# Optimization experiments

Hardware: AMD Instinct MI355X
Metric: run time of the kernel (lower is better)

## Reference

```python
import jax, jax.numpy as jnp
import numpy as np
import math

DIM = 512
HEADS = 8
DIM_HEAD = DIM // HEADS
TIME_DIM = 512
EPS = 1e-5


def _ln(x, g, b):
    m = jnp.mean(x, axis=-1, keepdims=True)
    v = jnp.var(x, axis=-1, keepdims=True)
    return (x - m) * jax.lax.rsqrt(v + EPS) * g + b


def setup_inputs() -> dict:
    key = jax.random.key(0)
    ks = jax.random.split(key, 16)
    s = 0.02
    return {
        "con_features": jax.random.normal(ks[0], (4, 1024, DIM), jnp.float32),
        "diff_features": jax.random.normal(ks[1], (4, 1024, DIM), jnp.float32),
        "time_emb": jax.random.normal(ks[2], (4, TIME_DIM), jnp.float32),
        "ln_con_g": jnp.ones((DIM,), jnp.float32),
        "ln_con_b": jnp.zeros((DIM,), jnp.float32),
        "ln_diff_g": jnp.ones((DIM,), jnp.float32),
        "ln_diff_b": jnp.zeros((DIM,), jnp.float32),
        "wq": jax.random.normal(ks[3], (DIM, DIM), jnp.float32) * s,
        "wk": jax.random.normal(ks[4], (DIM, DIM), jnp.float32) * s,
        "wv": jax.random.normal(ks[5], (DIM, DIM), jnp.float32) * s,
        "w_out": jax.random.normal(ks[6], (DIM, DIM), jnp.float32) * s,
        "b_out": jnp.zeros((DIM,), jnp.float32),
        "w_emd1": jax.random.normal(ks[7], (TIME_DIM, 2 * DIM), jnp.float32) * s,
        "b_emd1": jnp.zeros((2 * DIM,), jnp.float32),
        "w_emd2": jax.random.normal(ks[8], (2 * DIM, 2 * DIM), jnp.float32) * s,
        "b_emd2": jnp.zeros((2 * DIM,), jnp.float32),
        "mlp_ln_g": jnp.ones((DIM,), jnp.float32),
        "mlp_ln_b": jnp.zeros((DIM,), jnp.float32),
        "mlp_w1": jax.random.normal(ks[9], (DIM, DIM), jnp.float32) * s,
        "mlp_b1": jnp.zeros((DIM,), jnp.float32),
        "mlp_w2": jax.random.normal(ks[10], (DIM, DIM), jnp.float32) * s,
        "mlp_b2": jnp.zeros((DIM,), jnp.float32),
    }


def reference(con_features, diff_features, time_emb,
              ln_con_g, ln_con_b, ln_diff_g, ln_diff_b,
              wq, wk, wv, w_out, b_out,
              w_emd1, b_emd1, w_emd2, b_emd2,
              mlp_ln_g, mlp_ln_b, mlp_w1, mlp_b1, mlp_w2, mlp_b2):
    b, n, _ = diff_features.shape
    fea_q = _ln(diff_features, ln_diff_g, ln_diff_b)
    fea_kv = _ln(con_features, ln_con_g, ln_con_b)
    # projections (no bias) + split heads: b n (h d) -> b h n d
    def heads(x):
        return x.reshape(b, n, HEADS, DIM_HEAD).transpose(0, 2, 1, 3)
    q = heads(fea_q @ wq)
    k = heads(fea_kv @ wk)
    v = heads(fea_kv @ wv)
    # 2D FFT over (n, d), ortho norm
    qf = jnp.fft.fft2(q, axes=(-2, -1), norm="ortho")
    kf = jnp.fft.fft2(k, axes=(-2, -1), norm="ortho")
    dots = jnp.einsum("bhnd,bhmd->bhnm", qf, jnp.conj(kf))  # q @ k^H
    attn_c = jnp.fft.ifft2(dots, axes=(-2, -1), norm="ortho")
    mag = jnp.sqrt(attn_c.real ** 2 + attn_c.imag ** 2)
    attn = jax.nn.softmax(mag, axis=-1) / math.sqrt(DIM_HEAD)
    out = jnp.einsum("bhnm,bhmd->bhnd", attn, v)
    out = out.transpose(0, 2, 1, 3).reshape(b, n, DIM)  # b h n d -> b n (h d)
    # global per-sample normalization over (n, dim); torch.std uses ddof=1
    mu = jnp.mean(out, axis=(-2, -1), keepdims=True)
    sd = jnp.std(out, axis=(-2, -1), keepdims=True, ddof=1)
    out1 = (out - mu) / sd
    # FiLM from time embedding
    t = jax.nn.silu(time_emb @ w_emd1 + b_emd1)
    t = t @ w_emd2 + b_emd2
    mean_t, std_t = jnp.split(t, 2, axis=-1)
    out1 = out1 * std_t[:, None, :] + mean_t[:, None, :]
    out1 = out1 @ w_out + b_out
    # FeedForward: LN -> Linear -> GELU(exact) -> Linear
    h = _ln(out1, mlp_ln_g, mlp_ln_b)
    h = jax.nn.gelu(h @ mlp_w1 + mlp_b1, approximate=False)
    return h @ mlp_w2 + mlp_b2
```

## Files before the change

### kernel.cpp

```cpp
#include <hip/hip_runtime.h>
#include <math.h>


typedef _Float16 f16;
typedef _Float16 f16x8 __attribute__((ext_vector_type(8)));
typedef float f32x4 __attribute__((ext_vector_type(4)));

#define ROWS 4096
#define NTOK 1024
#define NB   4
#define NH   8
#define DH   64

struct PrepArgs { const float* src[6]; f16* dst[6]; };

__global__ __launch_bounds__(256) void k_prep(PrepArgs pa, float* stats,
                                              const float* b_emd1, const float* b_emd2,
                                              float* tbacc, float* filmp) {
    __shared__ float tile[32][33];
    int m = blockIdx.z;
    const float* src = pa.src[m];
    f16* dst = pa.dst[m];
    int i0 = blockIdx.y * 32;
    int o0 = blockIdx.x * 32;
    for (int r = threadIdx.y; r < 32; r += 8)
        tile[r][threadIdx.x] = src[(i0 + r) * 512 + o0 + threadIdx.x];
    __syncthreads();
    for (int r = threadIdx.y; r < 32; r += 8)
        dst[(o0 + r) * 512 + i0 + threadIdx.x] = (f16)tile[threadIdx.x][r];
    if (m == 0 && blockIdx.x == 0 && blockIdx.y == 0 && threadIdx.y == 0 && threadIdx.x < 8)
        stats[threadIdx.x] = 0.f;
    if (m == 0 && blockIdx.y == 1) {
        int o = blockIdx.x * 256 + threadIdx.y * 32 + threadIdx.x;
        tbacc[o] = b_emd1[o & 1023];
        filmp[o] = b_emd2[o & 1023];
    }
}

__global__ __launch_bounds__(256) void k_ln(const float* __restrict__ x0, const float* __restrict__ g0,
                                            const float* __restrict__ b0, f16* __restrict__ o0,
                                            const float* __restrict__ x1, const float* __restrict__ g1,
                                            const float* __restrict__ b1, f16* __restrict__ o1,
                                            int n0) {
    int wid = threadIdx.x >> 6, lane = threadIdx.x & 63;
    long row = (long)blockIdx.x * 4 + wid;
    const float *x, *g, *bb; f16* o;
    if (row < n0) { x = x0 + row * 512; g = g0; bb = b0; o = o0 + row * 512; }
    else { long r = row - n0; x = x1 + r * 512; g = g1; bb = b1; o = o1 + r * 512; }
    float v[8]; float s = 0.f;
#pragma unroll
    for (int j = 0; j < 8; j++) { v[j] = x[lane + 64 * j]; s += v[j]; }
#pragma unroll
    for (int d = 32; d >= 1; d >>= 1) s += __shfl_xor(s, d, 64);
    float mean = s * (1.f / 512.f);
    float q = 0.f;
#pragma unroll
    for (int j = 0; j < 8; j++) { float t = v[j] - mean; q += t * t; }
#pragma unroll
    for (int d = 32; d >= 1; d >>= 1) q += __shfl_xor(q, d, 64);
    float inv = rsqrtf(q * (1.f / 512.f) + 1e-5f);
#pragma unroll
    for (int j = 0; j < 8; j++) {
        int c = lane + 64 * j;
        o[c] = (f16)((v[j] - mean) * inv * g[c] + bb[c]);
    }
}

__global__ __launch_bounds__(256) void k_film1s(const float* __restrict__ temb, const float* __restrict__ w1,
                                                float* __restrict__ tbacc) {
    __shared__ float tsh[4][32];
    int tid = threadIdx.x;
    int c = blockIdx.x * 256 + tid;
    int k0 = blockIdx.y * 32;
    if (tid < 128) tsh[tid >> 5][tid & 31] = temb[(tid >> 5) * 512 + k0 + (tid & 31)];
    __syncthreads();
    float a0 = 0.f, a1 = 0.f, a2 = 0.f, a3 = 0.f;
#pragma unroll 8
    for (int k = 0; k < 32; k++) {
        float w = w1[(k0 + k) * 1024 + c];
        a0 += tsh[0][k] * w; a1 += tsh[1][k] * w; a2 += tsh[2][k] * w; a3 += tsh[3][k] * w;
    }
    atomicAdd(&tbacc[c], a0);        atomicAdd(&tbacc[1024 + c], a1);
    atomicAdd(&tbacc[2048 + c], a2); atomicAdd(&tbacc[3072 + c], a3);
}

__global__ __launch_bounds__(256) void k_film2s(const float* __restrict__ tbacc, const float* __restrict__ w2,
                                                float* __restrict__ filmp) {
    __shared__ float tsh[4][32];
    int tid = threadIdx.x;
    int c = blockIdx.x * 256 + tid;
    int k0 = blockIdx.y * 32;
    if (tid < 128) {
        float v = tbacc[(tid >> 5) * 1024 + k0 + (tid & 31)];
        tsh[tid >> 5][tid & 31] = v / (1.f + __expf(-v));
    }
    __syncthreads();
    float a0 = 0.f, a1 = 0.f, a2 = 0.f, a3 = 0.f;
#pragma unroll 8
    for (int k = 0; k < 32; k++) {
        float w = w2[(k0 + k) * 1024 + c];
        a0 += tsh[0][k] * w; a1 += tsh[1][k] * w; a2 += tsh[2][k] * w; a3 += tsh[3][k] * w;
    }
    atomicAdd(&filmp[c], a0);        atomicAdd(&filmp[1024 + c], a1);
    atomicAdd(&filmp[2048 + c], a2); atomicAdd(&filmp[3072 + c], a3);
}

__global__ __launch_bounds__(256) void k_qkv(const f16* __restrict__ A16, const f16* __restrict__ C16,
                                             const f16* __restrict__ wqT, const f16* __restrict__ wkT,
                                             const f16* __restrict__ wvT,
                                             f16* __restrict__ Qh, f16* __restrict__ Kh, f16* __restrict__ Vt) {
    __shared__ f16 Ash[128][72];
    __shared__ f16 Bsh[64][72];
    const int z = blockIdx.z;
    const f16* A  = (z == 0) ? A16 : C16;
    const f16* BT = (z == 0) ? wqT : (z == 1) ? wkT : wvT;
    const int tid = threadIdx.x;
    const int lane = tid & 63, wid = tid >> 6;
    const int quad = lane >> 4, l15 = lane & 15;
    const int m0 = blockIdx.y * 128, n0 = blockIdx.x * 64;
    const int wm = (wid >> 1) * 64, wn = (wid & 1) * 32;
    f32x4 acc[4][2] = {};
    for (int kk = 0; kk < 512; kk += 64) {
#pragma unroll
        for (int p = 0; p < 4; p++) {
            int c = tid + p * 256;
            int r = c >> 3, cc = (c & 7) * 8;
            *(f16x8*)&Ash[r][cc] = *(const f16x8*)&A[(long)(m0 + r) * 512 + kk + cc];
        }
#pragma unroll
        for (int p = 0; p < 2; p++) {
            int c = tid + p * 256;
            int r = c >> 3, cc = (c & 7) * 8;
            *(f16x8*)&Bsh[r][cc] = *(const f16x8*)&BT[(long)(n0 + r) * 512 + kk + cc];
        }
        __syncthreads();
#pragma unroll
        for (int ks = 0; ks < 2; ks++) {
            f16x8 af[4], bf[2];
#pragma unroll
            for (int t = 0; t < 4; t++)
                af[t] = *(const f16x8*)&Ash[wm + t * 16 + l15][ks * 32 + quad * 8];
#pragma unroll
            for (int t = 0; t < 2; t++)
                bf[t] = *(const f16x8*)&Bsh[wn + t * 16 + l15][ks * 32 + quad * 8];
#pragma unroll
            for (int mt = 0; mt < 4; mt++)
#pragma unroll
                for (int nt = 0; nt < 2; nt++)
                    acc[mt][nt] = __builtin_amdgcn_mfma_f32_16x16x32_f16(af[mt], bf[nt], acc[mt][nt], 0, 0, 0);
        }
        __syncthreads();
    }
    f16* qk = (z == 0) ? Qh : Kh;
#pragma unroll
    for (int mt = 0; mt < 4; mt++)
#pragma unroll
        for (int nt = 0; nt < 2; nt++)
#pragma unroll
            for (int r = 0; r < 4; r++) {
                int gm = m0 + wm + mt * 16 + quad * 4 + r;
                int gn = n0 + wn + nt * 16 + l15;
                float v = acc[mt][nt][r];
                int b = gm >> 10, n = gm & 1023, h = gn >> 6, d = gn & 63;
                if (z <= 1) {
                    qk[(((long)(b * NH + h)) * NTOK + n) * DH + d] = (f16)v;
                } else {
                    int nf = (NTOK - n) & (NTOK - 1);
                    Vt[(((long)(b * NH + h)) * DH + d) * NTOK + nf] = (f16)v;
                }
            }
}

template <int EPI>
__global__ __launch_bounds__(256) void k_gemm64(const f16* __restrict__ A, const f16* __restrict__ BT,
                                                const float* __restrict__ bias, void* __restrict__ dstv) {
    __shared__ f16 Ash[64][72];
    __shared__ f16 Bsh[64][72];
    const int tid = threadIdx.x;
    const int lane = tid & 63, wid = tid >> 6;
    const int quad = lane >> 4, l15 = lane & 15;
    const int m0 = blockIdx.y * 64, n0 = blockIdx.x * 64;
    const int wm = (wid >> 1) * 32, wn = (wid & 1) * 32;
    f32x4 acc[2][2] = {};
    for (int kk = 0; kk < 512; kk += 64) {
#pragma unroll
        for (int p = 0; p < 2; p++) {
            int c = tid + p * 256;
            int r = c >> 3, cc = (c & 7) * 8;
            *(f16x8*)&Ash[r][cc] = *(const f16x8*)&A[(long)(m0 + r) * 512 + kk + cc];
            *(f16x8*)&Bsh[r][cc] = *(const f16x8*)&BT[(long)(n0 + r) * 512 + kk + cc];
        }
        __syncthreads();
#pragma unroll
        for (int ks = 0; ks < 2; ks++) {
            f16x8 af[2], bf[2];
#pragma unroll
            for (int t = 0; t < 2; t++) {
                af[t] = *(const f16x8*)&Ash[wm + t * 16 + l15][ks * 32 + quad * 8];
                bf[t] = *(const f16x8*)&Bsh[wn + t * 16 + l15][ks * 32 + quad * 8];
            }
#pragma unroll
            for (int mt = 0; mt < 2; mt++)
#pragma unroll
                for (int nt = 0; nt < 2; nt++)
                    acc[mt][nt] = __builtin_amdgcn_mfma_f32_16x16x32_f16(af[mt], bf[nt], acc[mt][nt], 0, 0, 0);
        }
        __syncthreads();
    }
#pragma unroll
    for (int mt = 0; mt < 2; mt++)
#pragma unroll
        for (int nt = 0; nt < 2; nt++)
#pragma unroll
            for (int r = 0; r < 4; r++) {
                int gm = m0 + wm + mt * 16 + quad * 4 + r;
                int gn = n0 + wn + nt * 16 + l15;
                float v = acc[mt][nt][r];
                if (EPI == 3) {
                    float x = v + bias[gn];
                    ((f16*)dstv)[(long)gm * 512 + gn] = (f16)(0.5f * x * (1.0f + erff(x * 0.70710678f)));
                } else {
                    ((float*)dstv)[(long)gm * 512 + gn] = v + bias[gn];
                }
            }
}

__global__ __launch_bounds__(256) void k_attn(const f16* __restrict__ Q, const f16* __restrict__ K,
                                              const f16* __restrict__ Vt, float* __restrict__ out,
                                              float* __restrict__ stats) {
    __shared__ f16 Ksh[128][72];
    __shared__ f16 Vsh[80][136];
    __shared__ f16 Psh[4][16][136];
    __shared__ float rbuf[8];
    const int tid = threadIdx.x, lane = tid & 63, wid = tid >> 6;
    const int quad = lane >> 4, l15 = lane & 15;
    const int bh = blockIdx.x;
    const int b = bh >> 3, h = bh & 7, q0 = blockIdx.y * 64;
    const f16* Qbh = Q + (long)bh * NTOK * DH;
    const f16* Kbh = K + (long)bh * NTOK * DH;
    const f16* Vbh = Vt + (long)bh * DH * NTOK;
    for (int i = tid; i < 16 * 136; i += 256) {
        int r = i / 136, c = i - r * 136;
        Vsh[64 + r][c] = (f16)((r == 0) ? 1.f : 0.f);
    }
    const int qrow = q0 + wid * 16 + l15;
    f16x8 qf[2];
    qf[0] = *(const f16x8*)&Qbh[(long)qrow * DH + quad * 8];
    qf[1] = *(const f16x8*)&Qbh[(long)qrow * DH + 32 + quad * 8];
    f32x4 O[5] = {};

    for (int k0 = 0; k0 < NTOK; k0 += 128) {
        __syncthreads();
#pragma unroll
        for (int p = 0; p < 4; p++) {
            int c = tid + p * 256;
            int r = c >> 3, cc = (c & 7) * 8;
            *(f16x8*)&Ksh[r][cc] = *(const f16x8*)&Kbh[(long)(k0 + r) * DH + cc];
        }
#pragma unroll
        for (int p = 0; p < 4; p++) {
            int c = tid + p * 256;
            int r = c >> 4, cc = (c & 15) * 8;
            *(f16x8*)&Vsh[r][cc] = *(const f16x8*)&Vbh[(long)r * NTOK + k0 + cc];
        }
        __syncthreads();
        f32x4 S[8] = {};
#pragma unroll
        for (int ks = 0; ks < 2; ks++)
#pragma unroll
            for (int nt = 0; nt < 8; nt++) {
                f16x8 kf = *(const f16x8*)&Ksh[nt * 16 + l15][ks * 32 + quad * 8];
                S[nt] = __builtin_amdgcn_mfma_f32_16x16x32_f16(qf[ks], kf, S[nt], 0, 0, 0);
            }
#pragma unroll
        for (int nt = 0; nt < 8; nt++)
#pragma unroll
            for (int r = 0; r < 4; r++) {
                float p = __expf(fminf(fabsf(S[nt][r]) - 8.f, 11.f));
                Psh[wid][quad * 4 + r][nt * 16 + l15] = (f16)p;
            }
#pragma unroll
        for (int ks = 0; ks < 4; ks++) {
            f16x8 pf = *(const f16x8*)&Psh[wid][l15][ks * 32 + quad * 8];
#pragma unroll
            for (int vt = 0; vt < 5; vt++) {
                f16x8 vf = *(const f16x8*)&Vsh[vt * 16 + l15][ks * 32 + quad * 8];
                O[vt] = __builtin_amdgcn_mfma_f32_16x16x32_f16(pf, vf, O[vt], 0, 0, 0);
            }
        }
    }
    float lb[4];
#pragma unroll
    for (int r = 0; r < 4; r++) lb[r] = 0.125f / __shfl(O[4][r], lane & 48, 64);
    float lsum = 0.f, lsq = 0.f;
#pragma unroll
    for (int t = 0; t < 4; t++)
#pragma unroll
        for (int r = 0; r < 4; r++) {
            float v = O[t][r] * lb[r];
            int gn = q0 + wid * 16 + quad * 4 + r;
            int gc = h * DH + t * 16 + l15;
            out[((long)b * NTOK + gn) * 512 + gc] = v;
            lsum += v; lsq += v * v;
        }
#pragma unroll
    for (int d = 32; d >= 1; d >>= 1) { lsum += __shfl_xor(lsum, d, 64); lsq += __shfl_xor(lsq, d, 64); }
    if (lane == 0) { rbuf[wid] = lsum; rbuf[4 + wid] = lsq; }
    __syncthreads();
    if (tid == 0) {
        atomicAdd(&stats[b * 2], rbuf[0] + rbuf[1] + rbuf[2] + rbuf[3]);
        atomicAdd(&stats[b * 2 + 1], rbuf[4] + rbuf[5] + rbuf[6] + rbuf[7]);
    }
}

__global__ __launch_bounds__(256) void k_film_apply(const float* __restrict__ ao, const float* __restrict__ stats,
                                                    const float* __restrict__ filmp, f16* __restrict__ x2) {
    long base = ((long)blockIdx.x * 256 + threadIdx.x) * 4;
    int b = (int)(base >> 19);
    float sum = stats[b * 2], sq = stats[b * 2 + 1];
    const float M = 524288.f;
    float mu = sum / M;
    float var = (sq - sum * mu) / (M - 1.f);
    float isd = rsqrtf(var);
    int c = (int)(base & 511);
    float4 v = *(const float4*)&ao[base];
    float mt[4], st[4];
#pragma unroll
    for (int j = 0; j < 4; j++) { mt[j] = filmp[b * 1024 + c + j]; st[j] = filmp[b * 1024 + 512 + c + j]; }
    x2[base + 0] = (f16)(((v.x - mu) * isd) * st[0] + mt[0]);
    x2[base + 1] = (f16)(((v.y - mu) * isd) * st[1] + mt[1]);
    x2[base + 2] = (f16)(((v.z - mu) * isd) * st[2] + mt[2]);
    x2[base + 3] = (f16)(((v.w - mu) * isd) * st[3] + mt[3]);
}

extern "C" void kernel_launch(void* const* d_in, const int* in_sizes, int n_in,
                              void* d_out, int out_size, void* d_ws, size_t ws_size,
                              hipStream_t stream) {
    const float* con      = (const float*)d_in[0];
    const float* diff     = (const float*)d_in[1];
    const float* temb     = (const float*)d_in[2];
    const float* ln_con_g = (const float*)d_in[3];
    const float* ln_con_b = (const float*)d_in[4];
    const float* ln_dif_g = (const float*)d_in[5];
    const float* ln_dif_b = (const float*)d_in[6];
    const float* wq       = (const float*)d_in[7];
    const float* wk       = (const float*)d_in[8];
    const float* wv       = (const float*)d_in[9];
    const float* w_out    = (const float*)d_in[10];
    const float* b_out    = (const float*)d_in[11];
    const float* w_emd1   = (const float*)d_in[12];
    const float* b_emd1   = (const float*)d_in[13];
    const float* w_emd2   = (const float*)d_in[14];
    const float* b_emd2   = (const float*)d_in[15];
    const float* mlp_ln_g = (const float*)d_in[16];
    const float* mlp_ln_b = (const float*)d_in[17];
    const float* mlp_w1   = (const float*)d_in[18];
    const float* mlp_b1   = (const float*)d_in[19];
    const float* mlp_w2   = (const float*)d_in[20];
    const float* mlp_b2   = (const float*)d_in[21];
    float* outp = (float*)d_out;

    char* ws = (char*)d_ws;
    size_t off = 0;
    auto alloc = [&](size_t bytes) { void* p = ws + off; off += (bytes + 255) & ~(size_t)255; return p; };
    f16*   A16   = (f16*)alloc((size_t)ROWS * 512 * 2);
    f16*   C16   = (f16*)alloc((size_t)ROWS * 512 * 2);
    f16*   Qh    = (f16*)alloc((size_t)ROWS * 512 * 2);
    f16*   Kh    = (f16*)alloc((size_t)ROWS * 512 * 2);
    f16*   Vt    = (f16*)alloc((size_t)ROWS * 512 * 2);
    float* aout  = (float*)alloc((size_t)ROWS * 512 * 4);
    f16*   wqT   = (f16*)alloc(512 * 512 * 2);
    f16*   wkT   = (f16*)alloc(512 * 512 * 2);
    f16*   wvT   = (f16*)alloc(512 * 512 * 2);
    f16*   woT   = (f16*)alloc(512 * 512 * 2);
    f16*   w1T   = (f16*)alloc(512 * 512 * 2);
    f16*   w2T   = (f16*)alloc(512 * 512 * 2);
    float* tbacc = (float*)alloc(4 * 1024 * 4);
    float* filmp = (float*)alloc(4 * 1024 * 4);
    float* stats = (float*)alloc(256);
    float* out1  = (float*)Qh;
    f16*   X2    = Vt;
    f16*   X3    = A16;
    f16*   X4    = C16;

    PrepArgs pa;
    pa.src[0] = wq;  pa.src[1] = wk;  pa.src[2] = wv;
    pa.src[3] = w_out; pa.src[4] = mlp_w1; pa.src[5] = mlp_w2;
    pa.dst[0] = wqT; pa.dst[1] = wkT; pa.dst[2] = wvT;
    pa.dst[3] = woT; pa.dst[4] = w1T; pa.dst[5] = w2T;

    k_prep<<<dim3(16, 16, 6), dim3(32, 8), 0, stream>>>(pa, stats, b_emd1, b_emd2, tbacc, filmp);
    k_film1s<<<dim3(4, 16), dim3(256), 0, stream>>>(temb, w_emd1, tbacc);
    k_film2s<<<dim3(4, 32), dim3(256), 0, stream>>>(tbacc, w_emd2, filmp);
    k_ln<<<dim3(2048), dim3(256), 0, stream>>>(diff, ln_dif_g, ln_dif_b, A16,
                                               con, ln_con_g, ln_con_b, C16, ROWS);
    k_qkv<<<dim3(8, 32, 3), dim3(256), 0, stream>>>(A16, C16, wqT, wkT, wvT, Qh, Kh, Vt);
    k_attn<<<dim3(32, 16), dim3(256), 0, stream>>>(Qh, Kh, Vt, aout, stats);
    k_film_apply<<<dim3(2048), dim3(256), 0, stream>>>(aout, stats, filmp, X2);
    k_gemm64<2><<<dim3(8, 64), dim3(256), 0, stream>>>(X2, woT, b_out, (void*)out1);
    k_ln<<<dim3(1024), dim3(256), 0, stream>>>(out1, mlp_ln_g, mlp_ln_b, X3,
                                               out1, mlp_ln_g, mlp_ln_b, X3, ROWS);
    k_gemm64<3><<<dim3(8, 64), dim3(256), 0, stream>>>(X3, w1T, mlp_b1, (void*)X4);
    k_gemm64<4><<<dim3(8, 64), dim3(256), 0, stream>>>(X4, w2T, mlp_b2, (void*)outp);
}
```

Measured before the change: 210.0 us.

## Use direct global-to-LDS loads with XOR-swizzled tiles and coalesced QKV epilogue

Replaces the register-staged global loads in the QKV, generic GEMM and attention kernels with global_load_lds 16-byte transfers straight into shared memory. Tiles are unpadded, and an XOR swizzle on the column slot avoids bank conflicts. The QKV epilogue now stages results through LDS so that Q, K and transposed V are written to global memory as vectorized, coalesced rows. The token-index reversal moves from V to K. The aim is to cut VGPR traffic, drop one barrier per k-step and remove the scattered 2-byte stores, at the cost of more intricate indexing and a dependence on the row flip staying mathematically equivalent.

```diff
diff --git a/kernel.cpp b/kernel.cpp
--- a/kernel.cpp
+++ b/kernel.cpp
@@ -11,6 +11,11 @@
 #define NB   4
 #define NH   8
 #define DH   64
+
+__device__ __forceinline__ void glds16(const f16* g, f16* l) {
+    __builtin_amdgcn_global_load_lds((const __attribute__((address_space(1))) void*)g,
+                                     (__attribute__((address_space(3))) void*)l, 16, 0, 0);
+}
 
 struct PrepArgs { const float* src[6]; f16* dst[6]; };
 
@@ -108,9 +113,10 @@
 __global__ __launch_bounds__(256) void k_qkv(const f16* __restrict__ A16, const f16* __restrict__ C16,
                                              const f16* __restrict__ wqT, const f16* __restrict__ wkT,
                                              const f16* __restrict__ wvT,
-                                             f16* __restrict__ Qh, f16* __restrict__ Kh, f16* __restrict__ Vt) {
-    __shared__ f16 Ash[128][72];
-    __shared__ f16 Bsh[64][72];
+                                             f16* __restrict__ Qh, f16* __restrict__ Kf, f16* __restrict__ Vt) {
+    __shared__ __attribute__((aligned(16))) f16 sh[128 * 64 + 64 * 64];
+    f16* Ash = sh;
+    f16* Bsh = sh + 128 * 64;
     const int z = blockIdx.z;
     const f16* A  = (z == 0) ? A16 : C16;
     const f16* BT = (z == 0) ? wqT : (z == 1) ? wkT : wvT;
@@ -119,85 +125,108 @@
     const int quad = lane >> 4, l15 = lane & 15;
     const int m0 = blockIdx.y * 128, n0 = blockIdx.x * 64;
     const int wm = (wid >> 1) * 64, wn = (wid & 1) * 32;
+    const int rl = lane >> 3, jj = (lane & 7) ^ rl;
+    const int sA = ((lane & 7) ^ (l15 & 7)) * 8;
     f32x4 acc[4][2] = {};
     for (int kk = 0; kk < 512; kk += 64) {
-#pragma unroll
-        for (int p = 0; p < 4; p++) {
-            int c = tid + p * 256;
-            int r = c >> 3, cc = (c & 7) * 8;
-            *(f16x8*)&Ash[r][cc] = *(const f16x8*)&A[(long)(m0 + r) * 512 + kk + cc];
-        }
-#pragma unroll
-        for (int p = 0; p < 2; p++) {
-            int c = tid + p * 256;
-            int r = c >> 3, cc = (c & 7) * 8;
-            *(f16x8*)&Bsh[r][cc] = *(const f16x8*)&BT[(long)(n0 + r) * 512 + kk + cc];
+        if (kk) __syncthreads();
+#pragma unroll
+        for (int c = 0; c < 4; c++) {
+            int r = c * 32 + 8 * wid + rl;
+            glds16(&A[(long)(m0 + r) * 512 + kk + 8 * jj], &Ash[(c * 32 + 8 * wid) * 64]);
+        }
+#pragma unroll
+        for (int c = 0; c < 2; c++) {
+            int r = c * 32 + 8 * wid + rl;
+            glds16(&BT[(long)(n0 + r) * 512 + kk + 8 * jj], &Bsh[(c * 32 + 8 * wid) * 64]);
         }
         __syncthreads();
 #pragma unroll
         for (int ks = 0; ks < 2; ks++) {
+            const int slot = ((ks * 4 + quad) ^ (l15 & 7)) * 8;
             f16x8 af[4], bf[2];
 #pragma unroll
             for (int t = 0; t < 4; t++)
-                af[t] = *(const f16x8*)&Ash[wm + t * 16 + l15][ks * 32 + quad * 8];
+                af[t] = *(const f16x8*)&Ash[(wm + t * 16 + l15) * 64 + slot];
 #pragma unroll
             for (int t = 0; t < 2; t++)
-                bf[t] = *(const f16x8*)&Bsh[wn + t * 16 + l15][ks * 32 + quad * 8];
+                bf[t] = *(const f16x8*)&Bsh[(wn + t * 16 + l15) * 64 + slot];
 #pragma unroll
             for (int mt = 0; mt < 4; mt++)
 #pragma unroll
                 for (int nt = 0; nt < 2; nt++)
                     acc[mt][nt] = __builtin_amdgcn_mfma_f32_16x16x32_f16(af[mt], bf[nt], acc[mt][nt], 0, 0, 0);
         }
+    }
+    __syncthreads();
+    const int bb = m0 >> 10, nn0 = m0 & 1023, h = blockIdx.x;
+    if (z <= 1) {
+#pragma unroll
+        for (int mt = 0; mt < 4; mt++)
+#pragma unroll
+            for (int nt = 0; nt < 2; nt++)
+#pragma unroll
+                for (int r = 0; r < 4; r++)
+                    sh[(wm + mt * 16 + quad * 4 + r) * 72 + wn + nt * 16 + l15] = (f16)acc[mt][nt][r];
         __syncthreads();
-    }
-    f16* qk = (z == 0) ? Qh : Kh;
-#pragma unroll
-    for (int mt = 0; mt < 4; mt++)
-#pragma unroll
-        for (int nt = 0; nt < 2; nt++)
-#pragma unroll
-            for (int r = 0; r < 4; r++) {
-                int gm = m0 + wm + mt * 16 + quad * 4 + r;
-                int gn = n0 + wn + nt * 16 + l15;
-                float v = acc[mt][nt][r];
-                int b = gm >> 10, n = gm & 1023, h = gn >> 6, d = gn & 63;
-                if (z <= 1) {
-                    qk[(((long)(b * NH + h)) * NTOK + n) * DH + d] = (f16)v;
-                } else {
-                    int nf = (NTOK - n) & (NTOK - 1);
-                    Vt[(((long)(b * NH + h)) * DH + d) * NTOK + nf] = (f16)v;
-                }
-            }
+        f16* dst = (z == 0) ? Qh : Kf;
+        long basebh = ((long)(bb * NH + h)) * NTOK * DH;
+#pragma unroll
+        for (int q2 = 0; q2 < 4; q2++) {
+            int c = tid + q2 * 256;
+            int row = c >> 3, col = (c & 7) * 8;
+            int n = nn0 + row;
+            int nr = (z == 1) ? ((NTOK - n) & (NTOK - 1)) : n;
+            *(f16x8*)&dst[basebh + (long)nr * DH + col] = *(const f16x8*)&sh[row * 72 + col];
+        }
+    } else {
+#pragma unroll
+        for (int mt = 0; mt < 4; mt++)
+#pragma unroll
+            for (int nt = 0; nt < 2; nt++)
+#pragma unroll
+                for (int r = 0; r < 4; r++)
+                    sh[(wn + nt * 16 + l15) * 136 + wm + mt * 16 + quad * 4 + r] = (f16)acc[mt][nt][r];
+        __syncthreads();
+        long basev = ((long)(bb * NH + h)) * DH * NTOK;
+#pragma unroll
+        for (int q2 = 0; q2 < 4; q2++) {
+            int c = tid + q2 * 256;
+            int d = c >> 4, col = (c & 15) * 8;
+            *(f16x8*)&Vt[basev + (long)d * NTOK + nn0 + col] = *(const f16x8*)&sh[d * 136 + col];
+        }
+    }
 }
 
 template <int EPI>
 __global__ __launch_bounds__(256) void k_gemm64(const f16* __restrict__ A, const f16* __restrict__ BT,
                                                 const float* __restrict__ bias, void* __restrict__ dstv) {
-    __shared__ f16 Ash[64][72];
-    __shared__ f16 Bsh[64][72];
+    __shared__ __attribute__((aligned(16))) f16 Ash[64 * 64];
+    __shared__ __attribute__((aligned(16))) f16 Bsh[64 * 64];
     const int tid = threadIdx.x;
     const int lane = tid & 63, wid = tid >> 6;
     const int quad = lane >> 4, l15 = lane & 15;
     const int m0 = blockIdx.y * 64, n0 = blockIdx.x * 64;
     const int wm = (wid >> 1) * 32, wn = (wid & 1) * 32;
+    const int rl = lane >> 3, jj = (lane & 7) ^ rl;
     f32x4 acc[2][2] = {};
     for (int kk = 0; kk < 512; kk += 64) {
-#pragma unroll
-        for (int p = 0; p < 2; p++) {
-            int c = tid + p * 256;
-            int r = c >> 3, cc = (c & 7) * 8;
-            *(f16x8*)&Ash[r][cc] = *(const f16x8*)&A[(long)(m0 + r) * 512 + kk + cc];
-            *(f16x8*)&Bsh[r][cc] = *(const f16x8*)&BT[(long)(n0 + r) * 512 + kk + cc];
+        if (kk) __syncthreads();
+#pragma unroll
+        for (int c = 0; c < 2; c++) {
+            int r = c * 32 + 8 * wid + rl;
+            glds16(&A[(long)(m0 + r) * 512 + kk + 8 * jj], &Ash[(c * 32 + 8 * wid) * 64]);
+            glds16(&BT[(long)(n0 + r) * 512 + kk + 8 * jj], &Bsh[(c * 32 + 8 * wid) * 64]);
         }
         __syncthreads();
 #pragma unroll
         for (int ks = 0; ks < 2; ks++) {
+            const int slot = ((ks * 4 + quad) ^ (l15 & 7)) * 8;
             f16x8 af[2], bf[2];
 #pragma unroll
             for (int t = 0; t < 2; t++) {
-                af[t] = *(const f16x8*)&Ash[wm + t * 16 + l15][ks * 32 + quad * 8];
-                bf[t] = *(const f16x8*)&Bsh[wn + t * 16 + l15][ks * 32 + quad * 8];
+                af[t] = *(const f16x8*)&Ash[(wm + t * 16 + l15) * 64 + slot];
+                bf[t] = *(const f16x8*)&Bsh[(wn + t * 16 + l15) * 64 + slot];
             }
 #pragma unroll
             for (int mt = 0; mt < 2; mt++)
@@ -205,7 +234,6 @@
                 for (int nt = 0; nt < 2; nt++)
                     acc[mt][nt] = __builtin_amdgcn_mfma_f32_16x16x32_f16(af[mt], bf[nt], acc[mt][nt], 0, 0, 0);
         }
-        __syncthreads();
     }
 #pragma unroll
     for (int mt = 0; mt < 2; mt++)
@@ -225,23 +253,25 @@
             }
 }
 
-__global__ __launch_bounds__(256) void k_attn(const f16* __restrict__ Q, const f16* __restrict__ K,
+__global__ __launch_bounds__(256) void k_attn(const f16* __restrict__ Q, const f16* __restrict__ Kf,
                                               const f16* __restrict__ Vt, float* __restrict__ out,
                                               float* __restrict__ stats) {
-    __shared__ f16 Ksh[128][72];
-    __shared__ f16 Vsh[80][136];
-    __shared__ f16 Psh[4][16][136];
+    __shared__ __attribute__((aligned(16))) f16 Ksh[128 * 64];
+    __shared__ __attribute__((aligned(16))) f16 Vsh[80 * 128];
+    __shared__ __attribute__((aligned(16))) f16 Psh[4 * 16 * 136];
     __shared__ float rbuf[8];
     const int tid = threadIdx.x, lane = tid & 63, wid = tid >> 6;
     const int quad = lane >> 4, l15 = lane & 15;
     const int bh = blockIdx.x;
     const int b = bh >> 3, h = bh & 7, q0 = blockIdx.y * 64;
     const f16* Qbh = Q + (long)bh * NTOK * DH;
-    const f16* Kbh = K + (long)bh * NTOK * DH;
+    const f16* Kbh = Kf + (long)bh * NTOK * DH;
     const f16* Vbh = Vt + (long)bh * DH * NTOK;
-    for (int i = tid; i < 16 * 136; i += 256) {
-        int r = i / 136, c = i - r * 136;
-        Vsh[64 + r][c] = (f16)((r == 0) ? 1.f : 0.f);
+    const int rl = lane >> 3, jj8 = (lane & 7) ^ rl;
+    const int rl4 = lane >> 4, jjv = (lane & 15) ^ (4 * wid + rl4);
+    for (int i = tid; i < 16 * 128; i += 256) {
+        int r = i >> 7, c2 = i & 127;
+        Vsh[(64 + r) * 128 + c2] = (f16)((r == 0) ? 1.f : 0.f);
     }
     const int qrow = q0 + wid * 16 + l15;
     f16x8 qf[2];
@@ -250,41 +280,42 @@
     f32x4 O[5] = {};
 
     for (int k0 = 0; k0 < NTOK; k0 += 128) {
-        __syncthreads();
-#pragma unroll
-        for (int p = 0; p < 4; p++) {
-            int c = tid + p * 256;
-            int r = c >> 3, cc = (c & 7) * 8;
-            *(f16x8*)&Ksh[r][cc] = *(const f16x8*)&Kbh[(long)(k0 + r) * DH + cc];
-        }
-#pragma unroll
-        for (int p = 0; p < 4; p++) {
-            int c = tid + p * 256;
-            int r = c >> 4, cc = (c & 15) * 8;
-            *(f16x8*)&Vsh[r][cc] = *(const f16x8*)&Vbh[(long)r * NTOK + k0 + cc];
+        if (k0) __syncthreads();
+#pragma unroll
+        for (int c = 0; c < 4; c++) {
+            int rk = c * 32 + 8 * wid + rl;
+            glds16(&Kbh[(long)(k0 + rk) * DH + 8 * jj8], &Ksh[(c * 32 + 8 * wid) * 64]);
+        }
+#pragma unroll
+        for (int c = 0; c < 4; c++) {
+            int rv = c * 16 + 4 * wid + rl4;
+            glds16(&Vbh[(long)rv * NTOK + k0 + 8 * jjv], &Vsh[(c * 16 + 4 * wid) * 128]);
         }
         __syncthreads();
         f32x4 S[8] = {};
 #pragma unroll
-        for (int ks = 0; ks < 2; ks++)
+        for (int ks = 0; ks < 2; ks++) {
+            const int slot = ((ks * 4 + quad) ^ (l15 & 7)) * 8;
 #pragma unroll
             for (int nt = 0; nt < 8; nt++) {
-                f16x8 kf = *(const f16x8*)&Ksh[nt * 16 + l15][ks * 32 + quad * 8];
+                f16x8 kf = *(const f16x8*)&Ksh[(nt * 16 + l15) * 64 + slot];
                 S[nt] = __builtin_amdgcn_mfma_f32_16x16x32_f16(qf[ks], kf, S[nt], 0, 0, 0);
             }
+        }
 #pragma unroll
         for (int nt = 0; nt < 8; nt++)
 #pragma unroll
             for (int r = 0; r < 4; r++) {
                 float p = __expf(fminf(fabsf(S[nt][r]) - 8.f, 11.f));
-                Psh[wid][quad * 4 + r][nt * 16 + l15] = (f16)p;
+                Psh[(wid * 16 + quad * 4 + r) * 136 + nt * 16 + l15] = (f16)p;
             }
 #pragma unroll
         for (int ks = 0; ks < 4; ks++) {
-            f16x8 pf = *(const f16x8*)&Psh[wid][l15][ks * 32 + quad * 8];
+            f16x8 pf = *(const f16x8*)&Psh[(wid * 16 + l15) * 136 + ks * 32 + quad * 8];
+            const int vslot = ((ks * 4 + quad) ^ l15) * 8;
 #pragma unroll
             for (int vt = 0; vt < 5; vt++) {
-                f16x8 vf = *(const f16x8*)&Vsh[vt * 16 + l15][ks * 32 + quad * 8];
+                f16x8 vf = *(const f16x8*)&Vsh[(vt * 16 + l15) * 128 + vslot];
                 O[vt] = __builtin_amdgcn_mfma_f32_16x16x32_f16(pf, vf, O[vt], 0, 0, 0);
             }
         }
@@ -366,7 +397,7 @@
     f16*   A16   = (f16*)alloc((size_t)ROWS * 512 * 2);
     f16*   C16   = (f16*)alloc((size_t)ROWS * 512 * 2);
     f16*   Qh    = (f16*)alloc((size_t)ROWS * 512 * 2);
-    f16*   Kh    = (f16*)alloc((size_t)ROWS * 512 * 2);
+    f16*   Kf    = (f16*)alloc((size_t)ROWS * 512 * 2);
     f16*   Vt    = (f16*)alloc((size_t)ROWS * 512 * 2);
     float* aout  = (float*)alloc((size_t)ROWS * 512 * 4);
     f16*   wqT   = (f16*)alloc(512 * 512 * 2);
@@ -394,8 +425,8 @@
     k_film2s<<<dim3(4, 32), dim3(256), 0, stream>>>(tbacc, w_emd2, filmp);
     k_ln<<<dim3(2048), dim3(256), 0, stream>>>(diff, ln_dif_g, ln_dif_b, A16,
                                                con, ln_con_g, ln_con_b, C16, ROWS);
-    k_qkv<<<dim3(8, 32, 3), dim3(256), 0, stream>>>(A16, C16, wqT, wkT, wvT, Qh, Kh, Vt);
-    k_attn<<<dim3(32, 16), dim3(256), 0, stream>>>(Qh, Kh, Vt, aout, stats);
+    k_qkv<<<dim3(8, 32, 3), dim3(256), 0, stream>>>(A16, C16, wqT, wkT, wvT, Qh, Kf, Vt);
+    k_attn<<<dim3(32, 16), dim3(256), 0, stream>>>(Qh, Kf, Vt, aout, stats);
     k_film_apply<<<dim3(2048), dim3(256), 0, stream>>>(aout, stats, filmp, X2);
     k_gemm64<2><<<dim3(8, 64), dim3(256), 0, stream>>>(X2, woT, b_out, (void*)out1);
     k_ln<<<dim3(1024), dim3(256), 0, stream>>>(out1, mlp_ln_g, mlp_ln_b, X3,
```

New measurement: 196.5 us. -6.4%, faster.
